# Kernel optimization log

Measured on AMD Instinct MI355X. Metric: run time of the kernel, lower is better.

The kernel has to match this reference:

```python
import jax, jax.numpy as jnp
import numpy as np

# Social pooling hyperparameters (from init_kwargs config)
INFLUENCE_RADIUS = 10.0
SIGMA = 5.0
MAX_NEIGHBORS = 32
COORD_SCALE = 100.0  # coordinates uniform in [0, 100)^2


def setup_inputs() -> dict:
    key = jax.random.key(0)
    k1, k2 = jax.random.split(key)
    B, N, D = 8, 8192, 64
    features = jax.random.normal(k1, (B, N, D), dtype=jnp.float32)
    coordinates = jax.random.uniform(k2, (N, 2), dtype=jnp.float32) * COORD_SCALE
    return {"features": features, "coordinates": coordinates}


def _spatial_weights(coordinates):
    # Pairwise squared Euclidean distances [N, N]
    diff = coordinates[:, None, :] - coordinates[None, :, :]
    d2 = jnp.sum(diff * diff, axis=-1)
    d = jnp.sqrt(jnp.maximum(d2, 1e-12))
    # Gaussian kernel with hard radius cutoff
    w = jnp.exp(-d2 / (2.0 * SIGMA * SIGMA))
    w = jnp.where(d <= INFLUENCE_RADIUS, w, 0.0)
    # Neighbor limit: keep top-k weights per row
    topk_vals, _ = jax.lax.top_k(w, MAX_NEIGHBORS)  # [N, K]
    thresh = topk_vals[:, -1:]
    w = jnp.where(w >= thresh, w, 0.0)
    # weighted_mean normalization
    row_sums = jnp.clip(jnp.sum(w, axis=1, keepdims=True), 1e-8, None)
    return w / row_sums


def reference(features, coordinates):
    # features: [B, N, D]; coordinates: [N, 2]
    weights = _spatial_weights(coordinates)          # [N, N]
    pooled = jnp.einsum('ij,bjd->bid', weights, features)
    return pooled  # aggregation_layer is Identity (learnable_aggregation=False)
```

## Files before the change

### kernel.cpp

```cpp
#include <hip/hip_runtime.h>
#include <math.h>


constexpr int   NCELL  = 10;
constexpr int   NCELL2 = 100;
constexpr int   MAXC   = 448;
constexpr int   MAXK   = 64;
constexpr float BUCKSC = 2.56f;
constexpr int   NXCD   = 8;

__device__ __forceinline__ int cell_x(float x) {
    int c = (int)(x * 0.09765625f);
    return min(max(c, 0), NCELL - 1);
}
__device__ __forceinline__ int cell_of(float2 c) {
    return cell_x(c.y) * NCELL + cell_x(c.x);
}

__device__ __forceinline__ void wsync() {
    __builtin_amdgcn_wave_barrier();
    __threadfence_block();
    __builtin_amdgcn_wave_barrier();
}

__global__ __launch_bounds__(1024)
void k_prep(const float* __restrict__ C, int* __restrict__ cellStart,
            float2* __restrict__ bXY, int* __restrict__ bIdx, int N)
{
    __shared__ int h[NCELL2];
    __shared__ int cur[NCELL2];
    const int t = threadIdx.x;
    if (t < NCELL2) h[t] = 0;
    __syncthreads();
    const float2* C2 = (const float2*)C;
    for (int j = t; j < N; j += 1024) atomicAdd(&h[cell_of(C2[j])], 1);
    __syncthreads();
    if (t == 0) {
        int s = 0;
        for (int c = 0; c < NCELL2; ++c) { int n = h[c]; cur[c] = s; cellStart[c] = s; s += n; }
        cellStart[NCELL2] = s;
    }
    __syncthreads();
    for (int j = t; j < N; j += 1024) {
        float2 c = C2[j];
        int pos = atomicAdd(&cur[cell_of(c)], 1);
        bXY[pos] = c; bIdx[pos] = j;
    }
}

__global__ __launch_bounds__(256)
void social_pool_main(const float* __restrict__ F,
                      const float2* __restrict__ bXY,
                      const int* __restrict__ bIdx,
                      const int* __restrict__ cellStart,
                      float* __restrict__ out, int N, int B)
{
    __shared__ float s_cd2[4][MAXC];
    __shared__ int   s_cjj[4][MAXC];
    __shared__ __align__(16) int s_hist[4][256];
    __shared__ float s_blist[4][32];
    __shared__ float s_kw[4][MAXK];
    __shared__ int   s_kj[4][MAXK];

    const int t = threadIdx.x, wid = t >> 6, lane = t & 63;
    float* cd2   = s_cd2[wid];
    int*   cjj   = s_cjj[wid];
    int*   hist  = s_hist[wid];
    float* blist = s_blist[wid];
    float* kw    = s_kw[wid];
    int*   kj    = s_kj[wid];

    *(int4*)&hist[lane * 4] = make_int4(0, 0, 0, 0);

    const int bid = blockIdx.x, nb = gridDim.x;
    const int sb = (nb % NXCD == 0) ? (bid % NXCD) * (nb / NXCD) + bid / NXCD : bid;
    const int q = sb * 4 + wid;
    if (q >= N) return;

    const float2 ci = bXY[q];
    const int    i  = bIdx[q];
    const int cx = cell_x(ci.x), cy = cell_x(ci.y);
    const unsigned long long below = (1ull << lane) - 1ull;

    int mc = 0;
    for (int ry = max(cy - 1, 0); ry <= min(cy + 1, NCELL - 1); ++ry) {
        const int c0 = ry * NCELL + max(cx - 1, 0);
        const int c1 = ry * NCELL + min(cx + 1, NCELL - 1);
        const int s = cellStart[c0], e = cellStart[c1 + 1];
        for (int p0 = s; p0 < e; p0 += 64) {
            const int p = p0 + lane;
            bool hit = false; float d2 = 0.0f; int jj = 0;
            if (p < e) {
                float2 cp = bXY[p];
                float dx = ci.x - cp.x, dy = ci.y - cp.y;
                d2 = dx * dx + dy * dy;
                float d = sqrtf(fmaxf(d2, 1e-12f));
                if (d <= 10.0f) { hit = true; jj = bIdx[p]; }
            }
            unsigned long long mk = __ballot(hit);
            int off = __popcll(mk & below);
            if (hit && mc + off < MAXC) { cd2[mc + off] = d2; cjj[mc + off] = jj; }
            mc += (int)__popcll(mk);
        }
    }
    wsync();
    const int M = min(mc, MAXC);

    float thr_d2, thr_w;
    if (M > 32) {
        for (int k = lane; k < M; k += 64)
            atomicAdd(&hist[min(255, (int)(cd2[k] * BUCKSC))], 1);
        wsync();
        int4 h4 = *(const int4*)&hist[lane * 4];
        int hh0 = h4.x, hh1 = h4.y, hh2 = h4.z, hh3 = h4.w;
        int tot = hh0 + hh1 + hh2 + hh3;
        int sc = tot;
        #pragma unroll
        for (int o = 1; o < 64; o <<= 1) {
            int v = __shfl_up(sc, o);
            if (lane >= o) sc += v;
        }
        int ce = sc - tot;
        int fb = -1, fce = 0;
        if (ce <= 31 && 31 < ce + hh0) { fb = lane * 4 + 0; fce = ce; } ce += hh0;
        if (fb < 0 && ce <= 31 && 31 < ce + hh1) { fb = lane * 4 + 1; fce = ce; } ce += hh1;
        if (fb < 0 && ce <= 31 && 31 < ce + hh2) { fb = lane * 4 + 2; fce = ce; } ce += hh2;
        if (fb < 0 && ce <= 31 && 31 < ce + hh3) { fb = lane * 4 + 3; fce = ce; }
        unsigned long long mk1 = __ballot(fb >= 0);
        int src1 = (mk1 != 0ull) ? (__ffsll((unsigned long long)mk1) - 1) : 0;
        const int bstar   = __shfl(fb,  src1);
        const int cumexcl = __shfl(fce, src1);
        int bn = 0;
        for (int k0 = 0; k0 < M; k0 += 64) {
            const int k = k0 + lane;
            bool inb = (k < M) && (min(255, (int)(cd2[k] * BUCKSC)) == bstar);
            unsigned long long mk = __ballot(inb);
            int off = __popcll(mk & below);
            if (inb && bn + off < 32) blist[bn + off] = cd2[k];
            bn += (int)__popcll(mk);
        }
        wsync();
        bn = min(bn, 32);
        float mine = 0.0f; int ok = 0;
        if (lane < bn) {
            mine = blist[lane];
            int cl = 0, ceq = 0;
            for (int m = 0; m < bn; ++m) {
                cl  += (blist[m] <  mine);
                ceq += (blist[m] == mine);
            }
            int r = cumexcl + cl;
            ok = (r <= 31 && 31 < r + ceq);
        }
        unsigned long long mk2 = __ballot(ok);
        int src2 = (mk2 != 0ull) ? (__ffsll((unsigned long long)mk2) - 1) : 0;
        thr_d2 = __shfl(mine, src2);
        thr_w  = expf(-(thr_d2 / 50.0f));
    } else {
        thr_d2 = 3.4e38f;
        thr_w  = 0.0f;
    }

    const float marg = thr_d2 + 1e-4f;
    int kc = 0;
    for (int k0 = 0; k0 < M; k0 += 64) {
        const int k = k0 + lane;
        bool keep = false; float w = 0.0f; int jj = 0;
        if (k < M && cd2[k] <= marg) {
            w = expf(-(cd2[k] / 50.0f));
            if (w >= thr_w) { keep = true; jj = cjj[k]; }
        }
        unsigned long long mk = __ballot(keep);
        int off = __popcll(mk & below);
        if (keep && kc + off < MAXK) { kw[kc + off] = w; kj[kc + off] = jj; }
        kc += (int)__popcll(mk);
    }
    wsync();
    const int K = min(kc, MAXK);

    float v = (lane < K) ? kw[lane] : 0.0f;
    #pragma unroll
    for (int o = 32; o > 0; o >>= 1) v += __shfl_xor(v, o);
    const float ssum = fmaxf(v, 1e-8f);
    if (lane < K) kw[lane] = kw[lane] / ssum;
    wsync();

    const size_t NL = (size_t)N * 64;
    const float* F0 = F + lane;
    float* O0 = out + (size_t)i * 64 + lane;
    if (B == 8) {
        float a0=0,a1=0,a2=0,a3=0,a4=0,a5=0,a6=0,a7=0;
        for (int k = 0; k < K; ++k) {
            const float w = kw[k];
            const float* fp = F0 + (size_t)kj[k] * 64;
            a0 += w * fp[0*NL]; a1 += w * fp[1*NL];
            a2 += w * fp[2*NL]; a3 += w * fp[3*NL];
            a4 += w * fp[4*NL]; a5 += w * fp[5*NL];
            a6 += w * fp[6*NL]; a7 += w * fp[7*NL];
        }
        O0[0*NL]=a0; O0[1*NL]=a1; O0[2*NL]=a2; O0[3*NL]=a3;
        O0[4*NL]=a4; O0[5*NL]=a5; O0[6*NL]=a6; O0[7*NL]=a7;
    } else {
        for (int b = 0; b < B; ++b) {
            float a = 0.0f;
            const float* Fb = F0 + (size_t)b * NL;
            for (int k = 0; k < K; ++k)
                a += kw[k] * Fb[(size_t)kj[k] * 64];
            O0[(size_t)b * NL] = a;
        }
    }
}

extern "C" void kernel_launch(void* const* d_in, const int* in_sizes, int n_in,
                              void* d_out, int out_size, void* d_ws, size_t ws_size,
                              hipStream_t stream)
{
    const float* F = (const float*)d_in[0];
    const float* C = (const float*)d_in[1];
    float* out = (float*)d_out;

    const int N = in_sizes[1] / 2;
    const int B = in_sizes[0] / (N * 64);

    char* ws = (char*)d_ws;
    int*    cellStart = (int*)(ws + 0);
    float2* bXY       = (float2*)(ws + 512);
    int*    bIdx      = (int*)(ws + 512 + (size_t)N * 8);

    k_prep<<<1, 1024, 0, stream>>>(C, cellStart, bXY, bIdx, N);
    social_pool_main<<<(N + 3) / 4, 256, 0, stream>>>(F, bXY, bIdx, cellStart, out, N, B);
}
```

Baseline: 54.43 us.

## Vectorize gather with float4 loads, pack weights/indices, parallel prefix scan in prep

```diff
diff --git a/kernel.cpp b/kernel.cpp
--- a/kernel.cpp
+++ b/kernel.cpp
@@ -4,7 +4,7 @@
 
 constexpr int   NCELL  = 10;
 constexpr int   NCELL2 = 100;
-constexpr int   MAXC   = 448;
+constexpr int   MAXC   = 416;
 constexpr int   MAXK   = 64;
 constexpr float BUCKSC = 2.56f;
 constexpr int   NXCD   = 8;
@@ -27,18 +27,25 @@
 void k_prep(const float* __restrict__ C, int* __restrict__ cellStart,
             float2* __restrict__ bXY, int* __restrict__ bIdx, int N)
 {
-    __shared__ int h[NCELL2];
+    __shared__ int h[128];
     __shared__ int cur[NCELL2];
     const int t = threadIdx.x;
-    if (t < NCELL2) h[t] = 0;
+    if (t < 128) h[t] = 0;
     __syncthreads();
     const float2* C2 = (const float2*)C;
     for (int j = t; j < N; j += 1024) atomicAdd(&h[cell_of(C2[j])], 1);
     __syncthreads();
-    if (t == 0) {
-        int s = 0;
-        for (int c = 0; c < NCELL2; ++c) { int n = h[c]; cur[c] = s; cellStart[c] = s; s += n; }
-        cellStart[NCELL2] = s;
+    #pragma unroll
+    for (int o = 1; o < 128; o <<= 1) {
+        int u = (t < 128 && t >= o) ? h[t - o] : 0;
+        __syncthreads();
+        if (t < 128) h[t] += u;
+        __syncthreads();
+    }
+    if (t < NCELL2) {
+        int s = (t == 0) ? 0 : h[t - 1];
+        cur[t] = s; cellStart[t] = s;
+        if (t == 0) cellStart[NCELL2] = h[NCELL2 - 1];
     }
     __syncthreads();
     for (int j = t; j < N; j += 1024) {
@@ -48,27 +55,29 @@
     }
 }
 
-__global__ __launch_bounds__(256)
+template<int TN, int TB>
+__global__ __launch_bounds__(256, 8)
 void social_pool_main(const float* __restrict__ F,
                       const float2* __restrict__ bXY,
                       const int* __restrict__ bIdx,
                       const int* __restrict__ cellStart,
-                      float* __restrict__ out, int N, int B)
+                      float* __restrict__ out, int Nrt, int Brt)
 {
-    __shared__ float s_cd2[4][MAXC];
-    __shared__ int   s_cjj[4][MAXC];
+    const int N = (TN > 0) ? TN : Nrt;
+    const int B = (TB > 0) ? TB : Brt;
+
+    __shared__ float  s_cd2[4][MAXC];
+    __shared__ int    s_cjj[4][MAXC];
     __shared__ __align__(16) int s_hist[4][256];
-    __shared__ float s_blist[4][32];
-    __shared__ float s_kw[4][MAXK];
-    __shared__ int   s_kj[4][MAXK];
+    __shared__ float  s_blist[4][32];
+    __shared__ float2 s_kwj[4][MAXK];
 
     const int t = threadIdx.x, wid = t >> 6, lane = t & 63;
-    float* cd2   = s_cd2[wid];
-    int*   cjj   = s_cjj[wid];
-    int*   hist  = s_hist[wid];
-    float* blist = s_blist[wid];
-    float* kw    = s_kw[wid];
-    int*   kj    = s_kj[wid];
+    float*  cd2   = s_cd2[wid];
+    int*    cjj   = s_cjj[wid];
+    int*    hist  = s_hist[wid];
+    float*  blist = s_blist[wid];
+    float2* kwj   = s_kwj[wid];
 
     *(int4*)&hist[lane * 4] = make_int4(0, 0, 0, 0);
 
@@ -172,40 +181,51 @@
         }
         unsigned long long mk = __ballot(keep);
         int off = __popcll(mk & below);
-        if (keep && kc + off < MAXK) { kw[kc + off] = w; kj[kc + off] = jj; }
+        if (keep && kc + off < MAXK)
+            kwj[kc + off] = make_float2(w, __int_as_float(jj));
         kc += (int)__popcll(mk);
     }
     wsync();
     const int K = min(kc, MAXK);
 
-    float v = (lane < K) ? kw[lane] : 0.0f;
+    float v = (lane < K) ? kwj[lane].x : 0.0f;
     #pragma unroll
     for (int o = 32; o > 0; o >>= 1) v += __shfl_xor(v, o);
     const float ssum = fmaxf(v, 1e-8f);
-    if (lane < K) kw[lane] = kw[lane] / ssum;
+    if (lane < K) kwj[lane].x = kwj[lane].x / ssum;
     wsync();
 
     const size_t NL = (size_t)N * 64;
-    const float* F0 = F + lane;
-    float* O0 = out + (size_t)i * 64 + lane;
-    if (B == 8) {
-        float a0=0,a1=0,a2=0,a3=0,a4=0,a5=0,a6=0,a7=0;
+    if (TB == 8) {
+        const int dq = (lane & 15) * 4;
+        const int bp = (lane >> 4) * 2;
+        const float* Fb0 = F + (size_t)bp * NL + dq;
+        const float* Fb1 = Fb0 + NL;
+        float4 a0 = make_float4(0.f, 0.f, 0.f, 0.f);
+        float4 a1 = make_float4(0.f, 0.f, 0.f, 0.f);
+        #pragma unroll 2
         for (int k = 0; k < K; ++k) {
-            const float w = kw[k];
-            const float* fp = F0 + (size_t)kj[k] * 64;
-            a0 += w * fp[0*NL]; a1 += w * fp[1*NL];
-            a2 += w * fp[2*NL]; a3 += w * fp[3*NL];
-            a4 += w * fp[4*NL]; a5 += w * fp[5*NL];
-            a6 += w * fp[6*NL]; a7 += w * fp[7*NL];
-        }
-        O0[0*NL]=a0; O0[1*NL]=a1; O0[2*NL]=a2; O0[3*NL]=a3;
-        O0[4*NL]=a4; O0[5*NL]=a5; O0[6*NL]=a6; O0[7*NL]=a7;
+            float2 wj = kwj[k];
+            const float w = wj.x;
+            const size_t o = (size_t)__float_as_int(wj.y) * 64;
+            float4 f0 = *(const float4*)(Fb0 + o);
+            float4 f1 = *(const float4*)(Fb1 + o);
+            a0.x += w * f0.x; a0.y += w * f0.y; a0.z += w * f0.z; a0.w += w * f0.w;
+            a1.x += w * f1.x; a1.y += w * f1.y; a1.z += w * f1.z; a1.w += w * f1.w;
+        }
+        float* O0 = out + (size_t)bp * NL + (size_t)i * 64 + dq;
+        *(float4*)O0 = a0;
+        *(float4*)(O0 + NL) = a1;
     } else {
+        const float* F0 = F + lane;
+        float* O0 = out + (size_t)i * 64 + lane;
         for (int b = 0; b < B; ++b) {
             float a = 0.0f;
             const float* Fb = F0 + (size_t)b * NL;
-            for (int k = 0; k < K; ++k)
-                a += kw[k] * Fb[(size_t)kj[k] * 64];
+            for (int k = 0; k < K; ++k) {
+                float2 wj = kwj[k];
+                a += wj.x * Fb[(size_t)__float_as_int(wj.y) * 64];
+            }
             O0[(size_t)b * NL] = a;
         }
     }
@@ -228,5 +248,8 @@
     int*    bIdx      = (int*)(ws + 512 + (size_t)N * 8);
 
     k_prep<<<1, 1024, 0, stream>>>(C, cellStart, bXY, bIdx, N);
-    social_pool_main<<<(N + 3) / 4, 256, 0, stream>>>(F, bXY, bIdx, cellStart, out, N, B);
-}
+    if (N == 8192 && B == 8)
+        social_pool_main<8192, 8><<<2048, 256, 0, stream>>>(F, bXY, bIdx, cellStart, out, N, B);
+    else
+        social_pool_main<0, 0><<<(N + 3) / 4, 256, 0, stream>>>(F, bXY, bIdx, cellStart, out, N, B);
+}
```

After: 51.38 us. 5.6% less time.
